# Kernel optimization log

Measured on AMD Instinct MI355X. Metric: run time of the kernel, lower is better.

Reference implementation:

```python
import jax, jax.numpy as jnp
import numpy as np

N = 3  # lateral kernel size (hardcoded in original call via i:i+3 slices)


def _center_zero_mask(n, dtype):
    # ones everywhere except the center tap (the layer excludes self-connection)
    m = jnp.ones((n, n), dtype=dtype)
    return m.at[n // 2, n // 2].set(0.0)


def setup_inputs() -> dict:
    key = jax.random.key(0)
    kx, kk = jax.random.split(key)
    B, H, W, C = 32, 56, 56, 256
    x = jax.random.normal(kx, (B, H, W, C), dtype=jnp.float32)
    # glorot-ish scale for a (3,3,C) depthwise kernel
    kernel = jax.random.normal(kk, (N, N, C), dtype=jnp.float32) * 0.1
    return {"x": x, "kernel": kernel}


def reference(x, kernel):
    # x: [B,H,W,C], kernel: [n,n,C] (one n x n filter per channel)
    n, _, ch = kernel.shape
    masked = kernel * _center_zero_mask(n, kernel.dtype)[:, :, None]  # zero center tap
    # depthwise conv: HWIO with I=1, feature_group_count=C
    w = masked.reshape(n, n, 1, ch)
    out = jax.lax.conv_general_dilated(
        x, w,
        window_strides=(1, 1),
        padding="SAME",
        dimension_numbers=("NHWC", "HWIO", "NHWC"),
        feature_group_count=ch,
    )
    return out + x  # residual add
```

## Files before the change

kernel.cpp:

```cpp
#include <hip/hip_runtime.h>


#define BB 32
#define HH 56
#define WW 56
#define C4 64
#define NXCD 8
#define P 14
#define NHC 4
#define ROWSTR (WW * C4)

typedef float f32x4 __attribute__((ext_vector_type(4)));

__device__ __forceinline__ void ntstore4(const float4& v, float4* p) {
    __builtin_nontemporal_store(*(const f32x4*)&v, (f32x4*)p);
}

__device__ __forceinline__ void async16(const float4* g, float4* l) {
    __builtin_amdgcn_global_load_lds(
        (const __attribute__((address_space(1))) void*)g,
        (__attribute__((address_space(3))) void*)l,
        16, 0, 0);
}

#define WAITV2 asm volatile("s_waitcnt vmcnt(2)" ::: "memory")
#define WAITV6 asm volatile("s_waitcnt vmcnt(6)" ::: "memory")
#define WAITV8 asm volatile("s_waitcnt vmcnt(8)" ::: "memory")
#define LGKM0  asm volatile("s_waitcnt lgkmcnt(0)" ::: "memory")

#define CT(d, L, C, R)                                      \
    {                                                       \
        float4 K0 = kl[0*C4], K1 = kl[1*C4], K2 = kl[2*C4]; \
        (d).x = K0.x*(L).x + K1.x*(C).x + K2.x*(R).x;       \
        (d).y = K0.y*(L).y + K1.y*(C).y + K2.y*(R).y;       \
        (d).z = K0.z*(L).z + K1.z*(C).z + K2.z*(R).z;       \
        (d).w = K0.w*(L).w + K1.w*(C).w + K2.w*(R).w;       \
    }
#define AM(d, L, C, R)                                      \
    {                                                       \
        float4 K3 = kl[3*C4], K5 = kl[5*C4];                \
        (d).x += (C).x + K3.x*(L).x + K5.x*(R).x;           \
        (d).y += (C).y + K3.y*(L).y + K5.y*(R).y;           \
        (d).z += (C).z + K3.z*(L).z + K5.z*(R).z;           \
        (d).w += (C).w + K3.w*(L).w + K5.w*(R).w;           \
    }
#define AB(d, L, C, R)                                      \
    {                                                       \
        float4 K6 = kl[6*C4], K7 = kl[7*C4], K8 = kl[8*C4]; \
        (d).x += K6.x*(L).x + K7.x*(C).x + K8.x*(R).x;      \
        (d).y += K6.y*(L).y + K7.y*(C).y + K8.y*(R).y;      \
        (d).z += K6.z*(L).z + K7.z*(C).z + K8.z*(R).z;      \
        (d).w += K6.w*(L).w + K7.w*(C).w + K8.w*(R).w;      \
    }

#define READ2(slot)                                         \
    {                                                       \
        const float4* q = lrb + (slot) * 384;               \
        float4 a = q[lane],       bq = q[ 64+lane], cq = q[128+lane]; \
        float4 d = q[192+lane],   e  = q[256+lane], f  = q[320+lane]; \
        L0 = wl ? a : zero;  C0 = bq;  R0 = wr ? cq : zero; \
        L1 = wl ? d : zero;  C1 = e;   R1 = wr ? f  : zero; \
    }

#define STAGE2(ra, rb, slot)                                \
    {                                                       \
        int ya = (ra); ya = ya < 0 ? 0 : (ya > HH-1 ? HH-1 : ya); \
        int yb = (rb); yb = yb < 0 ? 0 : (yb > HH-1 ? HH-1 : yb); \
        const float4* pa = xim + (size_t)ya * ROWSTR;       \
        const float4* pb = xim + (size_t)yb * ROWSTR;       \
        float4* la = lrb + (slot) * 384;                    \
        async16(pa + oL, la);       async16(pa + oC, la +  64); \
        async16(pa + oR, la + 128); async16(pb + oL, la + 192); \
        async16(pb + oC, la + 256); async16(pb + oR, la + 320); \
    }

#define ROWFULL(L, C, R)                                    \
    {                                                       \
        AB(pA, L, C, R);                                    \
        ntstore4(pA, op); op += ROWSTR;                     \
        AM(pB, L, C, R);                                    \
        pA = pB;                                            \
        CT(pB, L, C, R);                                    \
    }

#define STEP2(slot, sra)                                    \
    {                                                       \
        WAITV8;                                             \
        READ2(slot);                                        \
        LGKM0;                                              \
        STAGE2((sra), (sra) + 1, slot);                     \
        ROWFULL(L0, C0, R0);                                \
        ROWFULL(L1, C1, R1);                                \
    }

__global__ __launch_bounds__(256, 4) void contour_kernel(
    const float4* __restrict__ x,
    const float4* __restrict__ kern,
    float4* __restrict__ out)
{
    __shared__ float4 lds_k[9 * C4];
    __shared__ float4 lds_rows[4][2][2][3][C4];
    for (int i = threadIdx.x; i < 9 * C4; i += 256)
        lds_k[i] = kern[i];
    __syncthreads();

    const int nblocks = gridDim.x;
    const int per_xcd = nblocks / NXCD;
    const int blk = (blockIdx.x % NXCD) * per_xcd + blockIdx.x / NXCD;

    const int lane = threadIdx.x & 63;
    const int wv   = threadIdx.x >> 6;
    int s  = (blk * 256 + threadIdx.x) >> 6;
    int w  = s % WW;
    int t  = s / WW;
    int hc = t & (NHC - 1);
    int b  = t >> 2;

    const float4 zero = make_float4(0.f, 0.f, 0.f, 0.f);
    const float4* kl  = lds_k + lane;
    float4*       lrb = &lds_rows[wv][0][0][0][0];

    const bool wl = (w > 0);
    const bool wr = (w < WW - 1);
    const int oC = w * C4 + lane;
    const int oL = (wl ? w - 1 : 0) * C4 + lane;
    const int oR = (wr ? w + 1 : WW - 1) * C4 + lane;

    const int h0 = hc * P;
    const float4* xim = x + (size_t)(b * HH) * ROWSTR;
    float4* op = out + (size_t)(b * HH + h0) * ROWSTR + w * C4 + lane;

    float4 L0, C0, R0, L1, C1, R1;
    float4 pA, pB;

    STAGE2(h0 - 1, h0,     0);
    STAGE2(h0 + 1, h0 + 2, 1);

    WAITV6;
    READ2(0);
    LGKM0;
    STAGE2(h0 + 3, h0 + 4, 0);
    if (h0 > 0) { CT(pB, L0, C0, R0); } else { pB = zero; }
    AM(pB, L1, C1, R1);
    pA = pB;
    CT(pB, L1, C1, R1);

    WAITV6;
    READ2(1);
    LGKM0;
    STAGE2(h0 + 5, h0 + 6, 1);
    ROWFULL(L0, C0, R0);
    ROWFULL(L1, C1, R1);

    int srow = h0 + 7;
    #pragma unroll 1
    for (int j = 0; j < 2; ++j) {
        STEP2(0, srow); srow += 2;
        STEP2(1, srow); srow += 2;
    }

    WAITV8;
    READ2(0);
    ROWFULL(L0, C0, R0);
    ROWFULL(L1, C1, R1);

    WAITV2;
    READ2(1);
    AB(pA, L0, C0, R0);
    ntstore4(pA, op); op += ROWSTR;
    AM(pB, L0, C0, R0);
    pA = pB;
    const bool hasbot = (h0 + P < HH);
    if (hasbot) { AB(pA, L1, C1, R1); }
    ntstore4(pA, op);
}

extern "C" void kernel_launch(void* const* d_in, const int* in_sizes, int n_in,
                              void* d_out, int out_size, void* d_ws, size_t ws_size,
                              hipStream_t stream) {
    const float4* x    = (const float4*)d_in[0];
    const float4* kern = (const float4*)d_in[1];
    float4* out        = (float4*)d_out;

    const int total = BB * NHC * WW * C4;
    const int block = 256;
    const int grid  = (total + block - 1) / block;
    contour_kernel<<<grid, block, 0, stream>>>(x, kern, out);
}
```

Baseline: 186.1 us.

## Share halo-column staging across the four waves of a block

Each block now handles four adjacent width columns, one per wave, instead of four unrelated columns. The waves jointly stage the six columns a row pair needs (four centres plus two halo columns) into one shared LDS buffer, so each thread issues three async loads per row pair instead of six. This removes redundant global and L2 reads of neighbouring columns. In exchange it adds block-wide barriers around every LDS read and retunes the vmcnt waits, which ties the four waves into lockstep and can expose load latency.

Measured after the change: 189.0 us. About the same (+1.5%).

```diff
diff --git a/kernel.cpp b/kernel.cpp
--- a/kernel.cpp
+++ b/kernel.cpp
@@ -24,9 +24,10 @@
 }
 
 #define WAITV2 asm volatile("s_waitcnt vmcnt(2)" ::: "memory")
-#define WAITV6 asm volatile("s_waitcnt vmcnt(6)" ::: "memory")
-#define WAITV8 asm volatile("s_waitcnt vmcnt(8)" ::: "memory")
+#define WAITV3 asm volatile("s_waitcnt vmcnt(3)" ::: "memory")
+#define WAITV5 asm volatile("s_waitcnt vmcnt(5)" ::: "memory")
 #define LGKM0  asm volatile("s_waitcnt lgkmcnt(0)" ::: "memory")
+#define BAR    __builtin_amdgcn_s_barrier()
 
 #define CT(d, L, C, R)                                      \
     {                                                       \
@@ -53,25 +54,26 @@
         (d).w += K6.w*(L).w + K7.w*(C).w + K8.w*(R).w;      \
     }
 
-#define READ2(slot)                                         \
-    {                                                       \
-        const float4* q = lrb + (slot) * 384;               \
-        float4 a = q[lane],       bq = q[ 64+lane], cq = q[128+lane]; \
-        float4 d = q[192+lane],   e  = q[256+lane], f  = q[320+lane]; \
+#define READ2C(slot)                                        \
+    {                                                       \
+        const float4* q = lrb + (slot)*768 + wv*64 + lane;  \
+        float4 a = q[0],   bq = q[64],  cq = q[128];        \
+        float4 d = q[384], e  = q[448], f  = q[512];        \
         L0 = wl ? a : zero;  C0 = bq;  R0 = wr ? cq : zero; \
         L1 = wl ? d : zero;  C1 = e;   R1 = wr ? f  : zero; \
     }
 
-#define STAGE2(ra, rb, slot)                                \
+#define STAGE2C(ra, rb, slot)                               \
     {                                                       \
         int ya = (ra); ya = ya < 0 ? 0 : (ya > HH-1 ? HH-1 : ya); \
         int yb = (rb); yb = yb < 0 ? 0 : (yb > HH-1 ? HH-1 : yb); \
-        const float4* pa = xim + (size_t)ya * ROWSTR;       \
-        const float4* pb = xim + (size_t)yb * ROWSTR;       \
-        float4* la = lrb + (slot) * 384;                    \
-        async16(pa + oL, la);       async16(pa + oC, la +  64); \
-        async16(pa + oR, la + 128); async16(pb + oL, la + 192); \
-        async16(pb + oC, la + 256); async16(pb + oR, la + 320); \
+        int y0 = rs0 ? yb : ya;                             \
+        int y1 = rs1 ? yb : ya;                             \
+        int y2 = rs2 ? yb : ya;                             \
+        float4* lb = lrb + (slot)*768;                      \
+        async16(xim + (size_t)y0*ROWSTR + gc0, lb + lo0);   \
+        async16(xim + (size_t)y1*ROWSTR + gc1, lb + lo1);   \
+        async16(xim + (size_t)y2*ROWSTR + gc2, lb + lo2);   \
     }
 
 #define ROWFULL(L, C, R)                                    \
@@ -81,16 +83,6 @@
         AM(pB, L, C, R);                                    \
         pA = pB;                                            \
         CT(pB, L, C, R);                                    \
-    }
-
-#define STEP2(slot, sra)                                    \
-    {                                                       \
-        WAITV8;                                             \
-        READ2(slot);                                        \
-        LGKM0;                                              \
-        STAGE2((sra), (sra) + 1, slot);                     \
-        ROWFULL(L0, C0, R0);                                \
-        ROWFULL(L1, C1, R1);                                \
     }
 
 __global__ __launch_bounds__(256, 4) void contour_kernel(
@@ -99,7 +91,7 @@
     float4* __restrict__ out)
 {
     __shared__ float4 lds_k[9 * C4];
-    __shared__ float4 lds_rows[4][2][2][3][C4];
+    __shared__ float4 lds_rows[2][2][6][C4];
     for (int i = threadIdx.x; i < 9 * C4; i += 256)
         lds_k[i] = kern[i];
     __syncthreads();
@@ -110,21 +102,33 @@
 
     const int lane = threadIdx.x & 63;
     const int wv   = threadIdx.x >> 6;
-    int s  = (blk * 256 + threadIdx.x) >> 6;
-    int w  = s % WW;
-    int t  = s / WW;
-    int hc = t & (NHC - 1);
-    int b  = t >> 2;
+    const int sblk = blk * 4;
+    const int w0   = sblk % WW;
+    const int tt   = sblk / WW;
+    const int hc   = tt & (NHC - 1);
+    const int b    = tt >> 2;
+    const int w    = w0 + wv;
 
     const float4 zero = make_float4(0.f, 0.f, 0.f, 0.f);
     const float4* kl  = lds_k + lane;
-    float4*       lrb = &lds_rows[wv][0][0][0][0];
+    float4*       lrb = &lds_rows[0][0][0][0];
 
     const bool wl = (w > 0);
     const bool wr = (w < WW - 1);
-    const int oC = w * C4 + lane;
-    const int oL = (wl ? w - 1 : 0) * C4 + lane;
-    const int oR = (wr ? w + 1 : WW - 1) * C4 + lane;
+
+    int rs0, rs1, rs2, gc0, gc1, gc2, lo0, lo1, lo2;
+    {
+        int p, c, wc;
+        p = wv*3 + 0; rs0 = (p >= 6); c = p - 6*rs0;
+        wc = w0 - 1 + c; wc = wc < 0 ? 0 : (wc > WW-1 ? WW-1 : wc);
+        gc0 = wc * C4 + lane; lo0 = rs0*384 + c*64;
+        p = wv*3 + 1; rs1 = (p >= 6); c = p - 6*rs1;
+        wc = w0 - 1 + c; wc = wc < 0 ? 0 : (wc > WW-1 ? WW-1 : wc);
+        gc1 = wc * C4 + lane; lo1 = rs1*384 + c*64;
+        p = wv*3 + 2; rs2 = (p >= 6); c = p - 6*rs2;
+        wc = w0 - 1 + c; wc = wc < 0 ? 0 : (wc > WW-1 ? WW-1 : wc);
+        gc2 = wc * C4 + lane; lo2 = rs2*384 + c*64;
+    }
 
     const int h0 = hc * P;
     const float4* xim = x + (size_t)(b * HH) * ROWSTR;
@@ -133,39 +137,50 @@
     float4 L0, C0, R0, L1, C1, R1;
     float4 pA, pB;
 
-    STAGE2(h0 - 1, h0,     0);
-    STAGE2(h0 + 1, h0 + 2, 1);
-
-    WAITV6;
-    READ2(0);
+    STAGE2C(h0 - 1, h0,     0);
+    STAGE2C(h0 + 1, h0 + 2, 1);
+
+    WAITV3;
+    BAR;
+    READ2C(0);
     LGKM0;
-    STAGE2(h0 + 3, h0 + 4, 0);
+    BAR;
     if (h0 > 0) { CT(pB, L0, C0, R0); } else { pB = zero; }
     AM(pB, L1, C1, R1);
     pA = pB;
     CT(pB, L1, C1, R1);
 
-    WAITV6;
-    READ2(1);
+    STAGE2C(h0 + 3, h0 + 4, 0);
+    WAITV3;
+    BAR;
+    READ2C(1);
     LGKM0;
-    STAGE2(h0 + 5, h0 + 6, 1);
+    BAR;
     ROWFULL(L0, C0, R0);
     ROWFULL(L1, C1, R1);
 
-    int srow = h0 + 7;
+    int sr = h0 + 5;
     #pragma unroll 1
     for (int j = 0; j < 2; ++j) {
-        STEP2(0, srow); srow += 2;
-        STEP2(1, srow); srow += 2;
-    }
-
-    WAITV8;
-    READ2(0);
+        STAGE2C(sr, sr + 1, 1); sr += 2;
+        WAITV5; BAR; READ2C(0); LGKM0; BAR;
+        ROWFULL(L0, C0, R0);
+        ROWFULL(L1, C1, R1);
+        STAGE2C(sr, sr + 1, 0); sr += 2;
+        WAITV5; BAR; READ2C(1); LGKM0; BAR;
+        ROWFULL(L0, C0, R0);
+        ROWFULL(L1, C1, R1);
+    }
+
+    STAGE2C(sr, sr + 1, 1);
+    WAITV5; BAR; READ2C(0); LGKM0; BAR;
     ROWFULL(L0, C0, R0);
     ROWFULL(L1, C1, R1);
 
     WAITV2;
-    READ2(1);
+    BAR;
+    READ2C(1);
+    LGKM0;
     AB(pA, L0, C0, R0);
     ntstore4(pA, op); op += ROWSTR;
     AM(pB, L0, C0, R0);
```
